# Performance work log

Measured on AMD Instinct MI355X. Metric: run time of the kernel, lower is better.

Reference implementation:

```python
import jax, jax.numpy as jnp
import numpy as np

N_NODES = 131072
N_EDGES = 2097152
N_GRAPHS = 2048
IN_CH, HID, OUT = 12, 64, 4


def gcn_conv(x, W, b, src, dst, n_nodes):
    """PyG GCNConv: out = D^{-1/2} (A + I) D^{-1/2} (x W) + b.
    Degree computed at target nodes including self loops (edge_weight=1)."""
    h = x @ W  # [N, F_out]
    # degree with self loops: in-degree + 1
    deg = jax.ops.segment_sum(jnp.ones((src.shape[0],), x.dtype), dst,
                              num_segments=n_nodes) + 1.0
    dinv = jax.lax.rsqrt(deg)  # [N]
    norm = dinv[src] * dinv[dst]  # [E]
    # scatter-add messages from src to dst
    agg = jax.ops.segment_sum(h[src] * norm[:, None], dst, num_segments=n_nodes)
    # self-loop contribution: norm_ii = dinv[i]^2
    agg = agg + h * (dinv * dinv)[:, None]
    return agg + b


def global_mean_pool(x, batch, n_graphs):
    sums = jax.ops.segment_sum(x, batch, num_segments=n_graphs)
    cnt = jax.ops.segment_sum(jnp.ones((x.shape[0],), x.dtype), batch,
                              num_segments=n_graphs)
    return sums / jnp.maximum(cnt, 1.0)[:, None]


def setup_inputs() -> dict:
    key = jax.random.key(0)
    ks = jax.random.split(key, 9)
    x = jax.random.normal(ks[0], (N_NODES, IN_CH), dtype=jnp.float32)
    edge_index = jax.random.randint(ks[1], (2, N_EDGES), 0, N_NODES, dtype=jnp.int64)
    batch = jnp.sort(jax.random.randint(ks[2], (N_NODES,), 0, N_GRAPHS, dtype=jnp.int64))
    def glorot(k, shape):
        lim = np.sqrt(6.0 / (shape[0] + shape[1]))
        return jax.random.uniform(k, shape, jnp.float32, -lim, lim)
    return {
        "x": x,
        "edge_index": edge_index,
        "batch": batch,
        "W1": glorot(ks[3], (IN_CH, HID)),
        "b1": jnp.zeros((HID,), jnp.float32),
        "W2": glorot(ks[4], (HID, HID)),
        "b2": jnp.zeros((HID,), jnp.float32),
        "Wfc": glorot(ks[5], (HID, OUT)),
        "bfc": jnp.zeros((OUT,), jnp.float32),
    }


def reference(x, edge_index, batch, W1, b1, W2, b2, Wfc, bfc):
    src, dst = edge_index[0], edge_index[1]
    h = jax.nn.relu(gcn_conv(x, W1, b1, src, dst, N_NODES))
    h = jax.nn.relu(gcn_conv(h, W2, b2, src, dst, N_NODES))
    g = global_mean_pool(h, batch, N_GRAPHS)  # [n_graphs, HID]
    return jax.nn.sigmoid(g @ Wfc + bfc)  # [n_graphs, OUT]
```

## Files before the change

### kernel.cpp

```cpp
#include <hip/hip_runtime.h>
#include <hip/hip_bf16.h>


#define N_NODES 131072
#define N_EDGES 2097152
#define N_GRAPHS 2048
#define IN_CH 12
#define HID 64
#define OUT_CH 4
#define NBUCK 512
#define CHUNK 8192
#define STRIDE 4608
#define CSR_STRIDE 5120
#define CAP 5120

typedef float f32x2 __attribute__((ext_vector_type(2)));

__device__ __forceinline__ unsigned short f2bf(float f) {
    unsigned u = __float_as_uint(f);
    return (unsigned short)((u + 0x7fffu + ((u >> 16) & 1u)) >> 16);
}
__device__ __forceinline__ unsigned pack2bf(float lo, float hi) {
    return (unsigned)f2bf(lo) | ((unsigned)f2bf(hi) << 16);
}
__device__ __forceinline__ float bflo(unsigned v) { return __uint_as_float(v << 16); }
__device__ __forceinline__ float bfhi(unsigned v) { return __uint_as_float(v & 0xFFFF0000u); }

__global__ __launch_bounds__(1024, 4)
void bucket_kernel(const int* __restrict__ src, const int* __restrict__ dst,
                   int* __restrict__ bucket_count, int* __restrict__ staged) {
    __shared__ int hist[NBUCK];
    __shared__ int lscan[NBUCK];
    __shared__ int gbase[NBUCK];
    __shared__ int cursor[NBUCK];
    __shared__ int sorted[CHUNK];
    int tid = threadIdx.x;
    int base = blockIdx.x * CHUNK;
    if (tid < NBUCK) { hist[tid] = 0; cursor[tid] = 0; }
    __syncthreads();
    int d8[8], s8[8];
#pragma unroll
    for (int k = 0; k < 8; k++) {
        int i = base + k * 1024 + tid;
        d8[k] = dst[i];
        s8[k] = src[i];
        atomicAdd(&hist[d8[k] >> 8], 1);
    }
    __syncthreads();
    if (tid < NBUCK) lscan[tid] = hist[tid];
    __syncthreads();
    for (int off = 1; off < NBUCK; off <<= 1) {
        int u = (tid < NBUCK && tid >= off) ? lscan[tid - off] : 0;
        __syncthreads();
        if (tid < NBUCK) lscan[tid] += u;
        __syncthreads();
    }
    if (tid < NBUCK) gbase[tid] = atomicAdd(&bucket_count[tid], hist[tid]);
    __syncthreads();
#pragma unroll
    for (int k = 0; k < 8; k++) {
        int b = d8[k] >> 8;
        int start = lscan[b] - hist[b];
        int p = start + atomicAdd(&cursor[b], 1);
        sorted[p] = ((d8[k] & 255) << 17) | s8[k];
    }
    __syncthreads();
    int wid = tid >> 6, lane = tid & 63;
    int g16 = lane >> 4, k16 = lane & 15;
    for (int b0 = wid * 4; b0 < NBUCK; b0 += 64) {
        int b = b0 + g16;
        int cb = hist[b];
        int lbase = lscan[b] - cb;
        int gb = b * STRIDE + gbase[b];
        for (int k = k16; k < cb; k += 16) staged[gb + k] = sorted[lbase + k];
    }
}

__global__ void build_kernel(const int* __restrict__ bucket_count, const int* __restrict__ staged,
                             int2* __restrict__ rowbounds, float* __restrict__ dinv,
                             int* __restrict__ csr, const float* __restrict__ x,
                             unsigned short* __restrict__ xb) {
    __shared__ int sl[STRIDE];
    __shared__ int image[CAP];
    __shared__ int cnt[256];
    __shared__ int scn[256];
    __shared__ int loff[256];
    __shared__ int cursor[256];
    __shared__ int totalS;
    int b = blockIdx.x;
    int tid = threadIdx.x;
    int count = bucket_count[b];
    const int* st = staged + b * STRIDE;
    cnt[tid] = 0;
    cursor[tid] = 0;
    for (int i = tid; i < count; i += 256) sl[i] = st[i];
    __syncthreads();
    for (int i = tid; i < count; i += 256) atomicAdd(&cnt[(sl[i] >> 17) & 255], 1);
    __syncthreads();
    int deg = cnt[tid];
    int degp = (deg + 3) & ~3;
    scn[tid] = degp;
    __syncthreads();
    for (int off = 1; off < 256; off <<= 1) {
        int u = (tid >= off) ? scn[tid - off] : 0;
        __syncthreads();
        scn[tid] += u;
        __syncthreads();
    }
    int lo = scn[tid] - degp;
    loff[tid] = lo;
    int nbase = (b << 8) + tid;
    int gb = b * CSR_STRIDE;
    rowbounds[nbase] = make_int2(gb + lo, gb + lo + degp);
    float dv = rsqrtf((float)deg + 1.0f);
    dinv[nbase] = dv;
    if (tid == 255) totalS = lo + degp;
    {
        const float* xp = x + nbase * IN_CH;
        unsigned o[8];
#pragma unroll
        for (int k = 0; k < 6; k++) o[k] = pack2bf(dv * xp[2 * k], dv * xp[2 * k + 1]);
        o[6] = 0; o[7] = 0;
        uint4* dstp = (uint4*)(xb + nbase * 16);
        dstp[0] = make_uint4(o[0], o[1], o[2], o[3]);
        dstp[1] = make_uint4(o[4], o[5], o[6], o[7]);
    }
    if (b == 0 && tid < 2)
        ((uint4*)(xb + (size_t)N_NODES * 16))[tid] = make_uint4(0, 0, 0, 0);
    __syncthreads();
    for (int i = tid; i < count; i += 256) {
        int rec = sl[i];
        int s = rec & 0x1FFFF;
        int dq = (rec >> 17) & 255;
        int p = loff[dq] + atomicAdd(&cursor[dq], 1);
        int val = s << 6;
        if (p < CAP) image[p] = val;
        else csr[gb + p] = val;
    }
    __syncthreads();
    int padval = N_NODES << 6;
    for (int p = loff[tid] + deg; p < loff[tid] + degp; p++) {
        if (p < CAP) image[p] = padval;
        else csr[gb + p] = padval;
    }
    __syncthreads();
    int lim = totalS < CAP ? totalS : CAP;
    int* dstp = csr + gb;
    for (int i = tid; i < lim; i += 256) dstp[i] = image[i];
}

__global__ void agg_x_kernel(const int2* __restrict__ rowbounds, const int* __restrict__ csr,
                             const float* __restrict__ dinv,
                             const unsigned short* __restrict__ xb, float* __restrict__ aggx) {
    int tid = threadIdx.x;
    int w = tid >> 6, lane = tid & 63, sub = lane >> 1, p = lane & 1;
    int qoff = 8 * p;
    int node = (blockIdx.x * 4 + w) * 32 + sub;
    int2 rb = rowbounds[node];
    float dn = dinv[node];
    f32x2 a0[4] = {{0, 0}, {0, 0}, {0, 0}, {0, 0}};
    f32x2 a1[4] = {{0, 0}, {0, 0}, {0, 0}, {0, 0}};
    f32x2 a2[4] = {{0, 0}, {0, 0}, {0, 0}, {0, 0}};
    f32x2 a3[4] = {{0, 0}, {0, 0}, {0, 0}, {0, 0}};
    for (int j = rb.x; j < rb.y; j += 4) {
        int4 e = *(const int4*)(csr + j);
        uint4 u0 = *(const uint4*)(xb + (e.x >> 2) + qoff);
        uint4 u1 = *(const uint4*)(xb + (e.y >> 2) + qoff);
        uint4 u2 = *(const uint4*)(xb + (e.z >> 2) + qoff);
        uint4 u3 = *(const uint4*)(xb + (e.w >> 2) + qoff);
        a0[0] += (f32x2){bflo(u0.x), bfhi(u0.x)};
        a0[1] += (f32x2){bflo(u0.y), bfhi(u0.y)};
        a0[2] += (f32x2){bflo(u0.z), bfhi(u0.z)};
        a0[3] += (f32x2){bflo(u0.w), bfhi(u0.w)};
        a1[0] += (f32x2){bflo(u1.x), bfhi(u1.x)};
        a1[1] += (f32x2){bflo(u1.y), bfhi(u1.y)};
        a1[2] += (f32x2){bflo(u1.z), bfhi(u1.z)};
        a1[3] += (f32x2){bflo(u1.w), bfhi(u1.w)};
        a2[0] += (f32x2){bflo(u2.x), bfhi(u2.x)};
        a2[1] += (f32x2){bflo(u2.y), bfhi(u2.y)};
        a2[2] += (f32x2){bflo(u2.z), bfhi(u2.z)};
        a2[3] += (f32x2){bflo(u2.w), bfhi(u2.w)};
        a3[0] += (f32x2){bflo(u3.x), bfhi(u3.x)};
        a3[1] += (f32x2){bflo(u3.y), bfhi(u3.y)};
        a3[2] += (f32x2){bflo(u3.z), bfhi(u3.z)};
        a3[3] += (f32x2){bflo(u3.w), bfhi(u3.w)};
    }
    uint4 su = *(const uint4*)(xb + node * 16 + qoff);
    a0[0] += (f32x2){bflo(su.x), bfhi(su.x)};
    a0[1] += (f32x2){bflo(su.y), bfhi(su.y)};
    a0[2] += (f32x2){bflo(su.z), bfhi(su.z)};
    a0[3] += (f32x2){bflo(su.w), bfhi(su.w)};
    f32x2 nd = {dn, dn};
    f32x2 s0 = nd * ((a0[0] + a1[0]) + (a2[0] + a3[0]));
    f32x2 s1 = nd * ((a0[1] + a1[1]) + (a2[1] + a3[1]));
    f32x2 s2 = nd * ((a0[2] + a1[2]) + (a2[2] + a3[2]));
    f32x2 s3 = nd * ((a0[3] + a1[3]) + (a2[3] + a3[3]));
    float4 o0 = make_float4(s0[0], s0[1], s1[0], s1[1]);
    float4 o1 = make_float4(s2[0], s2[1], s3[0], s3[1]);
    *(float4*)(aggx + node * 16 + qoff) = o0;
    *(float4*)(aggx + node * 16 + qoff + 4) = o1;
}

__global__ void w1w2_kernel(const float* __restrict__ aggx, const float* __restrict__ W1,
                            const float* __restrict__ b1, const float* __restrict__ W2,
                            const float* __restrict__ dinv, unsigned int* __restrict__ hout) {
    __shared__ float sW1[IN_CH * HID];
    __shared__ float sW2[HID * HID];
    __shared__ float sA[256];
    __shared__ float sh1[16 * HID];
    int tid = threadIdx.x;
    for (int i = tid; i < IN_CH * HID; i += 256) sW1[i] = W1[i];
    for (int i = tid; i < HID * HID; i += 256) sW2[i] = W2[i];
    int node0 = blockIdx.x * 16;
    sA[tid] = aggx[node0 * 16 + tid];
    __syncthreads();
    int nl = tid >> 4, c4 = (tid & 15) * 4;
    float a0 = 0, a1 = 0, a2 = 0, a3 = 0;
#pragma unroll
    for (int k = 0; k < IN_CH; k++) {
        float av = sA[nl * 16 + k];
        const float* w = &sW1[k * HID + c4];
        a0 += av * w[0]; a1 += av * w[1]; a2 += av * w[2]; a3 += av * w[3];
    }
    const float* bb = &b1[c4];
    sh1[nl * HID + c4 + 0] = fmaxf(a0 + bb[0], 0.0f);
    sh1[nl * HID + c4 + 1] = fmaxf(a1 + bb[1], 0.0f);
    sh1[nl * HID + c4 + 2] = fmaxf(a2 + bb[2], 0.0f);
    sh1[nl * HID + c4 + 3] = fmaxf(a3 + bb[3], 0.0f);
    __syncthreads();
    float c0 = 0, c1 = 0, c2 = 0, c3 = 0;
#pragma unroll 8
    for (int k = 0; k < HID; k++) {
        float hv = sh1[nl * HID + k];
        float4 w = *(const float4*)&sW2[k * HID + c4];
        c0 += hv * w.x; c1 += hv * w.y; c2 += hv * w.z; c3 += hv * w.w;
    }
    float dv = dinv[node0 + nl];
    unsigned int packed = (unsigned int)__builtin_amdgcn_cvt_pk_fp8_f32(dv * c0, dv * c1, 0, false);
    packed = (unsigned int)__builtin_amdgcn_cvt_pk_fp8_f32(dv * c2, dv * c3, (int)packed, true);
    hout[((node0 + nl) * HID + c4) >> 2] = packed;
    if (blockIdx.x == 0 && tid < 16)
        hout[((size_t)N_NODES * HID >> 2) + tid] = 0;
}

__device__ __forceinline__ void add_fp8(f32x2* a, uint2 u) {
    a[0] += __builtin_amdgcn_cvt_pk_f32_fp8((int)u.x, false);
    a[1] += __builtin_amdgcn_cvt_pk_f32_fp8((int)u.x, true);
    a[2] += __builtin_amdgcn_cvt_pk_f32_fp8((int)u.y, false);
    a[3] += __builtin_amdgcn_cvt_pk_f32_fp8((int)u.y, true);
}

__device__ __forceinline__ void agg_body(int beg, int end, const int* __restrict__ csr,
                                         const unsigned char* __restrict__ h,
                                         int qoff, float* r) {
    f32x2 a0[4] = {{0, 0}, {0, 0}, {0, 0}, {0, 0}};
    f32x2 a1[4] = {{0, 0}, {0, 0}, {0, 0}, {0, 0}};
    f32x2 a2[4] = {{0, 0}, {0, 0}, {0, 0}, {0, 0}};
    f32x2 a3[4] = {{0, 0}, {0, 0}, {0, 0}, {0, 0}};
    int j = beg;
    for (; j + 8 <= end; j += 8) {
        int4 ea = *(const int4*)(csr + j);
        int4 eb = *(const int4*)(csr + j + 4);
        uint2 u0 = *(const uint2*)(h + ea.x + qoff);
        uint2 u1 = *(const uint2*)(h + ea.y + qoff);
        uint2 u2 = *(const uint2*)(h + ea.z + qoff);
        uint2 u3 = *(const uint2*)(h + ea.w + qoff);
        uint2 u4 = *(const uint2*)(h + eb.x + qoff);
        uint2 u5 = *(const uint2*)(h + eb.y + qoff);
        uint2 u6 = *(const uint2*)(h + eb.z + qoff);
        uint2 u7 = *(const uint2*)(h + eb.w + qoff);
        add_fp8(a0, u0); add_fp8(a1, u1); add_fp8(a2, u2); add_fp8(a3, u3);
        add_fp8(a0, u4); add_fp8(a1, u5); add_fp8(a2, u6); add_fp8(a3, u7);
    }
    if (j < end) {
        int4 ea = *(const int4*)(csr + j);
        uint2 u0 = *(const uint2*)(h + ea.x + qoff);
        uint2 u1 = *(const uint2*)(h + ea.y + qoff);
        uint2 u2 = *(const uint2*)(h + ea.z + qoff);
        uint2 u3 = *(const uint2*)(h + ea.w + qoff);
        add_fp8(a0, u0); add_fp8(a1, u1); add_fp8(a2, u2); add_fp8(a3, u3);
    }
#pragma unroll
    for (int k = 0; k < 4; k++) {
        f32x2 s = (a0[k] + a1[k]) + (a2[k] + a3[k]);
        r[2 * k] = s[0];
        r[2 * k + 1] = s[1];
    }
}

__global__ void agg_pool_kernel(const int2* __restrict__ rowbounds, const int* __restrict__ csr,
                                const float* __restrict__ dinv,
                                const unsigned char* __restrict__ h,
                                const float* __restrict__ b, const int* __restrict__ batch,
                                float* __restrict__ pool, float* __restrict__ gcnt) {
    __shared__ float red[32][HID];
    __shared__ int gids[32];
    int tid = threadIdx.x;
    int w = tid >> 6, lane = tid & 63, sub = lane >> 3, q = lane & 7;
    int qoff = 8 * q;
    int node = (blockIdx.x * 4 + w) * 8 + sub;
    int2 rb = rowbounds[node];
    float dn = dinv[node];
    float r[8];
    agg_body(rb.x, rb.y, csr, h, qoff, r);
    uint2 su = *(const uint2*)(h + node * HID + qoff);
    f32x2 s0 = __builtin_amdgcn_cvt_pk_f32_fp8((int)su.x, false);
    f32x2 s1 = __builtin_amdgcn_cvt_pk_f32_fp8((int)su.x, true);
    f32x2 s2 = __builtin_amdgcn_cvt_pk_f32_fp8((int)su.y, false);
    f32x2 s3 = __builtin_amdgcn_cvt_pk_f32_fp8((int)su.y, true);
    float4 b0 = *(const float4*)&b[qoff];
    float4 b1 = *(const float4*)&b[qoff + 4];
    float4 v0, v1;
    v0.x = fmaxf(dn * (r[0] + s0[0]) + b0.x, 0.0f);
    v0.y = fmaxf(dn * (r[1] + s0[1]) + b0.y, 0.0f);
    v0.z = fmaxf(dn * (r[2] + s1[0]) + b0.z, 0.0f);
    v0.w = fmaxf(dn * (r[3] + s1[1]) + b0.w, 0.0f);
    v1.x = fmaxf(dn * (r[4] + s2[0]) + b1.x, 0.0f);
    v1.y = fmaxf(dn * (r[5] + s2[1]) + b1.y, 0.0f);
    v1.z = fmaxf(dn * (r[6] + s3[0]) + b1.z, 0.0f);
    v1.w = fmaxf(dn * (r[7] + s3[1]) + b1.w, 0.0f);
    int nl = w * 8 + sub;
    *(float4*)&red[nl][qoff] = v0;
    *(float4*)&red[nl][qoff + 4] = v1;
    if (q == 0) gids[nl] = batch[node];
    __syncthreads();
    if (tid < 64) {
        int c = tid;
        float acc = 0.0f;
        int cur = gids[0], cnt = 0;
        for (int n = 0; n < 32; n++) {
            int g = gids[n];
            if (g != cur) {
                atomicAdd(&pool[cur * HID + c], acc);
                if (c == 0) atomicAdd(&gcnt[cur], (float)cnt);
                acc = 0.0f; cnt = 0; cur = g;
            }
            acc += red[n][c];
            cnt++;
        }
        atomicAdd(&pool[cur * HID + c], acc);
        if (c == 0) atomicAdd(&gcnt[cur], (float)cnt);
    }
}

__global__ void final_kernel(const float* __restrict__ pool, const float* __restrict__ gcnt,
                             const float* __restrict__ Wfc, const float* __restrict__ bfc,
                             float* __restrict__ out) {
    int idx = blockIdx.x * 256 + threadIdx.x;
    if (idx >= N_GRAPHS * OUT_CH) return;
    int g = idx >> 2, o = idx & 3;
    float inv = 1.0f / fmaxf(gcnt[g], 1.0f);
    float acc = bfc[o];
#pragma unroll
    for (int k = 0; k < HID; k++) acc += pool[g * HID + k] * inv * Wfc[k * OUT_CH + o];
    out[idx] = 1.0f / (1.0f + expf(-acc));
}

extern "C" void kernel_launch(void* const* d_in, const int* in_sizes, int n_in,
                              void* d_out, int out_size, void* d_ws, size_t ws_size,
                              hipStream_t stream) {
    const float* x   = (const float*)d_in[0];
    const int* eidx  = (const int*)d_in[1];
    const int* batch = (const int*)d_in[2];
    const float* W1  = (const float*)d_in[3];
    const float* b1  = (const float*)d_in[4];
    const float* W2  = (const float*)d_in[5];
    const float* b2  = (const float*)d_in[6];
    const float* Wfc = (const float*)d_in[7];
    const float* bfc = (const float*)d_in[8];
    float* out = (float*)d_out;

    const int* src = eidx;
    const int* dst = eidx + N_EDGES;

    unsigned char* hB = (unsigned char*)d_ws;
    int*   csr    = (int*)(hB + (size_t)(N_NODES + 1) * HID);
    int*   staged = csr + (size_t)NBUCK * CSR_STRIDE;
    float* dinv   = (float*)(staged + (size_t)NBUCK * STRIDE);
    int2*  rowbounds = (int2*)(dinv + N_NODES);
    int*   bucket_count = (int*)(rowbounds + N_NODES);
    float* pool   = (float*)(bucket_count + NBUCK);
    float* gcnt   = pool + N_GRAPHS * HID;
    unsigned short* xb = (unsigned short*)(gcnt + N_GRAPHS);
    float* aggx   = (float*)(xb + (size_t)(N_NODES + 1) * 16);

    hipMemsetAsync(bucket_count, 0, (size_t)NBUCK * 4, stream);
    hipMemsetAsync(pool, 0, (size_t)(N_GRAPHS * HID + N_GRAPHS) * 4, stream);

    bucket_kernel<<<N_EDGES / CHUNK, 1024, 0, stream>>>(src, dst, bucket_count, staged);
    build_kernel<<<NBUCK, 256, 0, stream>>>(bucket_count, staged, rowbounds, dinv, csr, x, xb);

    agg_x_kernel<<<N_NODES / 128, 256, 0, stream>>>(rowbounds, csr, dinv, xb, aggx);
    w1w2_kernel<<<N_NODES / 16, 256, 0, stream>>>(aggx, W1, b1, W2, dinv, (unsigned int*)hB);

    agg_pool_kernel<<<N_NODES / 32, 256, 0, stream>>>(rowbounds, csr, dinv, hB, b2, batch,
                                                      pool, gcnt);

    final_kernel<<<(N_GRAPHS * OUT_CH + 255) / 256, 256, 0, stream>>>(pool, gcnt, Wfc, bfc, out);
}
```

Before: 197.1 us.

## Split fp8 hidden features into two channel halves aggregated in separate passes

The second-layer fp8 feature matrix is stored as two 32-channel planes instead of one 64-channel row, and aggregation plus pooling runs as two passes, one per half. Each pass gathers from a 4 MB table rather than an 8 MB one, so the random neighbour gathers are meant to hit in cache more often. In exchange the CSR indices and row bounds are read twice, pool atomics are split across two launches, and there is an extra kernel launch.

```diff
diff --git a/kernel.cpp b/kernel.cpp
--- a/kernel.cpp
+++ b/kernel.cpp
@@ -203,7 +203,8 @@
 
 __global__ void w1w2_kernel(const float* __restrict__ aggx, const float* __restrict__ W1,
                             const float* __restrict__ b1, const float* __restrict__ W2,
-                            const float* __restrict__ dinv, unsigned int* __restrict__ hout) {
+                            const float* __restrict__ dinv,
+                            unsigned char* __restrict__ hBa, unsigned char* __restrict__ hBb) {
     __shared__ float sW1[IN_CH * HID];
     __shared__ float sW2[HID * HID];
     __shared__ float sA[256];
@@ -238,9 +239,12 @@
     float dv = dinv[node0 + nl];
     unsigned int packed = (unsigned int)__builtin_amdgcn_cvt_pk_fp8_f32(dv * c0, dv * c1, 0, false);
     packed = (unsigned int)__builtin_amdgcn_cvt_pk_fp8_f32(dv * c2, dv * c3, (int)packed, true);
-    hout[((node0 + nl) * HID + c4) >> 2] = packed;
-    if (blockIdx.x == 0 && tid < 16)
-        hout[((size_t)N_NODES * HID >> 2) + tid] = 0;
+    unsigned char* base = (c4 < 32) ? hBa : hBb;
+    *(unsigned int*)(base + (size_t)(node0 + nl) * 32 + (c4 & 31)) = packed;
+    if (blockIdx.x == 0 && tid < 8) {
+        ((unsigned int*)(hBa + (size_t)N_NODES * 32))[tid] = 0;
+        ((unsigned int*)(hBb + (size_t)N_NODES * 32))[tid] = 0;
+    }
 }
 
 __device__ __forceinline__ void add_fp8(f32x2* a, uint2 u) {
@@ -250,96 +254,88 @@
     a[3] += __builtin_amdgcn_cvt_pk_f32_fp8((int)u.y, true);
 }
 
-__device__ __forceinline__ void agg_body(int beg, int end, const int* __restrict__ csr,
-                                         const unsigned char* __restrict__ h,
-                                         int qoff, float* r) {
+__global__ void agg_pool_half_kernel(const int2* __restrict__ rowbounds,
+                                     const int* __restrict__ csr,
+                                     const float* __restrict__ dinv,
+                                     const unsigned char* __restrict__ h,
+                                     const float* __restrict__ b2,
+                                     const int* __restrict__ batch,
+                                     float* __restrict__ pool, float* __restrict__ gcnt,
+                                     int chan_off, int do_gcnt) {
+    __shared__ float red[64][32];
+    __shared__ int gids[64];
+    int tid = threadIdx.x;
+    int w = tid >> 6, lane = tid & 63, sub = lane >> 2, q = lane & 3;
+    int qoff = 8 * q;
+    int nl = w * 16 + sub;
+    int node = blockIdx.x * 64 + nl;
+    int2 rb = rowbounds[node];
+    float dn = dinv[node];
     f32x2 a0[4] = {{0, 0}, {0, 0}, {0, 0}, {0, 0}};
     f32x2 a1[4] = {{0, 0}, {0, 0}, {0, 0}, {0, 0}};
     f32x2 a2[4] = {{0, 0}, {0, 0}, {0, 0}, {0, 0}};
     f32x2 a3[4] = {{0, 0}, {0, 0}, {0, 0}, {0, 0}};
-    int j = beg;
-    for (; j + 8 <= end; j += 8) {
+    int j = rb.x;
+    for (; j + 8 <= rb.y; j += 8) {
         int4 ea = *(const int4*)(csr + j);
         int4 eb = *(const int4*)(csr + j + 4);
-        uint2 u0 = *(const uint2*)(h + ea.x + qoff);
-        uint2 u1 = *(const uint2*)(h + ea.y + qoff);
-        uint2 u2 = *(const uint2*)(h + ea.z + qoff);
-        uint2 u3 = *(const uint2*)(h + ea.w + qoff);
-        uint2 u4 = *(const uint2*)(h + eb.x + qoff);
-        uint2 u5 = *(const uint2*)(h + eb.y + qoff);
-        uint2 u6 = *(const uint2*)(h + eb.z + qoff);
-        uint2 u7 = *(const uint2*)(h + eb.w + qoff);
+        uint2 u0 = *(const uint2*)(h + (ea.x >> 1) + qoff);
+        uint2 u1 = *(const uint2*)(h + (ea.y >> 1) + qoff);
+        uint2 u2 = *(const uint2*)(h + (ea.z >> 1) + qoff);
+        uint2 u3 = *(const uint2*)(h + (ea.w >> 1) + qoff);
+        uint2 u4 = *(const uint2*)(h + (eb.x >> 1) + qoff);
+        uint2 u5 = *(const uint2*)(h + (eb.y >> 1) + qoff);
+        uint2 u6 = *(const uint2*)(h + (eb.z >> 1) + qoff);
+        uint2 u7 = *(const uint2*)(h + (eb.w >> 1) + qoff);
         add_fp8(a0, u0); add_fp8(a1, u1); add_fp8(a2, u2); add_fp8(a3, u3);
         add_fp8(a0, u4); add_fp8(a1, u5); add_fp8(a2, u6); add_fp8(a3, u7);
     }
-    if (j < end) {
+    if (j < rb.y) {
         int4 ea = *(const int4*)(csr + j);
-        uint2 u0 = *(const uint2*)(h + ea.x + qoff);
-        uint2 u1 = *(const uint2*)(h + ea.y + qoff);
-        uint2 u2 = *(const uint2*)(h + ea.z + qoff);
-        uint2 u3 = *(const uint2*)(h + ea.w + qoff);
+        uint2 u0 = *(const uint2*)(h + (ea.x >> 1) + qoff);
+        uint2 u1 = *(const uint2*)(h + (ea.y >> 1) + qoff);
+        uint2 u2 = *(const uint2*)(h + (ea.z >> 1) + qoff);
+        uint2 u3 = *(const uint2*)(h + (ea.w >> 1) + qoff);
         add_fp8(a0, u0); add_fp8(a1, u1); add_fp8(a2, u2); add_fp8(a3, u3);
     }
-#pragma unroll
-    for (int k = 0; k < 4; k++) {
-        f32x2 s = (a0[k] + a1[k]) + (a2[k] + a3[k]);
-        r[2 * k] = s[0];
-        r[2 * k + 1] = s[1];
-    }
-}
-
-__global__ void agg_pool_kernel(const int2* __restrict__ rowbounds, const int* __restrict__ csr,
-                                const float* __restrict__ dinv,
-                                const unsigned char* __restrict__ h,
-                                const float* __restrict__ b, const int* __restrict__ batch,
-                                float* __restrict__ pool, float* __restrict__ gcnt) {
-    __shared__ float red[32][HID];
-    __shared__ int gids[32];
-    int tid = threadIdx.x;
-    int w = tid >> 6, lane = tid & 63, sub = lane >> 3, q = lane & 7;
-    int qoff = 8 * q;
-    int node = (blockIdx.x * 4 + w) * 8 + sub;
-    int2 rb = rowbounds[node];
-    float dn = dinv[node];
-    float r[8];
-    agg_body(rb.x, rb.y, csr, h, qoff, r);
-    uint2 su = *(const uint2*)(h + node * HID + qoff);
-    f32x2 s0 = __builtin_amdgcn_cvt_pk_f32_fp8((int)su.x, false);
-    f32x2 s1 = __builtin_amdgcn_cvt_pk_f32_fp8((int)su.x, true);
-    f32x2 s2 = __builtin_amdgcn_cvt_pk_f32_fp8((int)su.y, false);
-    f32x2 s3 = __builtin_amdgcn_cvt_pk_f32_fp8((int)su.y, true);
-    float4 b0 = *(const float4*)&b[qoff];
-    float4 b1 = *(const float4*)&b[qoff + 4];
+    uint2 su = *(const uint2*)(h + (size_t)node * 32 + qoff);
+    add_fp8(a0, su);
+    f32x2 s0 = (a0[0] + a1[0]) + (a2[0] + a3[0]);
+    f32x2 s1 = (a0[1] + a1[1]) + (a2[1] + a3[1]);
+    f32x2 s2 = (a0[2] + a1[2]) + (a2[2] + a3[2]);
+    f32x2 s3 = (a0[3] + a1[3]) + (a2[3] + a3[3]);
+    float4 bb0 = *(const float4*)&b2[chan_off + qoff];
+    float4 bb1 = *(const float4*)&b2[chan_off + qoff + 4];
     float4 v0, v1;
-    v0.x = fmaxf(dn * (r[0] + s0[0]) + b0.x, 0.0f);
-    v0.y = fmaxf(dn * (r[1] + s0[1]) + b0.y, 0.0f);
-    v0.z = fmaxf(dn * (r[2] + s1[0]) + b0.z, 0.0f);
-    v0.w = fmaxf(dn * (r[3] + s1[1]) + b0.w, 0.0f);
-    v1.x = fmaxf(dn * (r[4] + s2[0]) + b1.x, 0.0f);
-    v1.y = fmaxf(dn * (r[5] + s2[1]) + b1.y, 0.0f);
-    v1.z = fmaxf(dn * (r[6] + s3[0]) + b1.z, 0.0f);
-    v1.w = fmaxf(dn * (r[7] + s3[1]) + b1.w, 0.0f);
-    int nl = w * 8 + sub;
+    v0.x = fmaxf(dn * s0[0] + bb0.x, 0.0f);
+    v0.y = fmaxf(dn * s0[1] + bb0.y, 0.0f);
+    v0.z = fmaxf(dn * s1[0] + bb0.z, 0.0f);
+    v0.w = fmaxf(dn * s1[1] + bb0.w, 0.0f);
+    v1.x = fmaxf(dn * s2[0] + bb1.x, 0.0f);
+    v1.y = fmaxf(dn * s2[1] + bb1.y, 0.0f);
+    v1.z = fmaxf(dn * s3[0] + bb1.z, 0.0f);
+    v1.w = fmaxf(dn * s3[1] + bb1.w, 0.0f);
     *(float4*)&red[nl][qoff] = v0;
     *(float4*)&red[nl][qoff + 4] = v1;
     if (q == 0) gids[nl] = batch[node];
     __syncthreads();
     if (tid < 64) {
-        int c = tid;
+        int half = tid >> 5, c = tid & 31;
+        int n0 = half * 32;
         float acc = 0.0f;
-        int cur = gids[0], cnt = 0;
-        for (int n = 0; n < 32; n++) {
+        int cur = gids[n0], cnt = 0;
+        for (int n = n0; n < n0 + 32; n++) {
             int g = gids[n];
             if (g != cur) {
-                atomicAdd(&pool[cur * HID + c], acc);
-                if (c == 0) atomicAdd(&gcnt[cur], (float)cnt);
+                atomicAdd(&pool[cur * HID + chan_off + c], acc);
+                if (do_gcnt && c == 0) atomicAdd(&gcnt[cur], (float)cnt);
                 acc = 0.0f; cnt = 0; cur = g;
             }
             acc += red[n][c];
             cnt++;
         }
-        atomicAdd(&pool[cur * HID + c], acc);
-        if (c == 0) atomicAdd(&gcnt[cur], (float)cnt);
+        atomicAdd(&pool[cur * HID + chan_off + c], acc);
+        if (do_gcnt && c == 0) atomicAdd(&gcnt[cur], (float)cnt);
     }
 }
 
@@ -373,8 +369,9 @@
     const int* src = eidx;
     const int* dst = eidx + N_EDGES;
 
-    unsigned char* hB = (unsigned char*)d_ws;
-    int*   csr    = (int*)(hB + (size_t)(N_NODES + 1) * HID);
+    unsigned char* hBa = (unsigned char*)d_ws;
+    unsigned char* hBb = hBa + (size_t)(N_NODES + 1) * 32;
+    int*   csr    = (int*)(hBb + (size_t)(N_NODES + 1) * 32);
     int*   staged = csr + (size_t)NBUCK * CSR_STRIDE;
     float* dinv   = (float*)(staged + (size_t)NBUCK * STRIDE);
     int2*  rowbounds = (int2*)(dinv + N_NODES);
@@ -391,10 +388,12 @@
     build_kernel<<<NBUCK, 256, 0, stream>>>(bucket_count, staged, rowbounds, dinv, csr, x, xb);
 
     agg_x_kernel<<<N_NODES / 128, 256, 0, stream>>>(rowbounds, csr, dinv, xb, aggx);
-    w1w2_kernel<<<N_NODES / 16, 256, 0, stream>>>(aggx, W1, b1, W2, dinv, (unsigned int*)hB);
-
-    agg_pool_kernel<<<N_NODES / 32, 256, 0, stream>>>(rowbounds, csr, dinv, hB, b2, batch,
-                                                      pool, gcnt);
+    w1w2_kernel<<<N_NODES / 16, 256, 0, stream>>>(aggx, W1, b1, W2, dinv, hBa, hBb);
+
+    agg_pool_half_kernel<<<N_NODES / 64, 256, 0, stream>>>(rowbounds, csr, dinv, hBa, b2,
+                                                           batch, pool, gcnt, 0, 1);
+    agg_pool_half_kernel<<<N_NODES / 64, 256, 0, stream>>>(rowbounds, csr, dinv, hBb, b2,
+                                                           batch, pool, gcnt, 32, 0);
 
     final_kernel<<<(N_GRAPHS * OUT_CH + 255) / 256, 256, 0, stream>>>(pool, gcnt, Wfc, bfc, out);
 }
```

New measurement: 211.0 us. 1.07x slower.

## Process 64 nodes per block in w1w2 kernel with register-tiled 4x4 matmul

Applied to the files above, without the earlier changes.

The dense W1/W2 kernel now handles 64 nodes per block instead of 16, so the shared-memory load of the W1/W2 weights is spread over four times as many nodes. Each thread computes a 4-node by 4-channel tile of the second matmul from float4 loads, and the hidden layer is stored transposed with padding to avoid bank conflicts. This reduces redundant weight staging and LDS traffic per FMA. In exchange it uses more shared memory per block and more registers, which may lower occupancy.

```diff
diff --git a/kernel.cpp b/kernel.cpp
--- a/kernel.cpp
+++ b/kernel.cpp
@@ -206,41 +206,68 @@
                             const float* __restrict__ dinv, unsigned int* __restrict__ hout) {
     __shared__ float sW1[IN_CH * HID];
     __shared__ float sW2[HID * HID];
-    __shared__ float sA[256];
-    __shared__ float sh1[16 * HID];
+    __shared__ float sA[64 * 17];
+    __shared__ float sh1t[HID * 65];
     int tid = threadIdx.x;
     for (int i = tid; i < IN_CH * HID; i += 256) sW1[i] = W1[i];
     for (int i = tid; i < HID * HID; i += 256) sW2[i] = W2[i];
-    int node0 = blockIdx.x * 16;
-    sA[tid] = aggx[node0 * 16 + tid];
-    __syncthreads();
-    int nl = tid >> 4, c4 = (tid & 15) * 4;
-    float a0 = 0, a1 = 0, a2 = 0, a3 = 0;
-#pragma unroll
-    for (int k = 0; k < IN_CH; k++) {
-        float av = sA[nl * 16 + k];
-        const float* w = &sW1[k * HID + c4];
-        a0 += av * w[0]; a1 += av * w[1]; a2 += av * w[2]; a3 += av * w[3];
-    }
-    const float* bb = &b1[c4];
-    sh1[nl * HID + c4 + 0] = fmaxf(a0 + bb[0], 0.0f);
-    sh1[nl * HID + c4 + 1] = fmaxf(a1 + bb[1], 0.0f);
-    sh1[nl * HID + c4 + 2] = fmaxf(a2 + bb[2], 0.0f);
-    sh1[nl * HID + c4 + 3] = fmaxf(a3 + bb[3], 0.0f);
-    __syncthreads();
-    float c0 = 0, c1 = 0, c2 = 0, c3 = 0;
-#pragma unroll 8
+    int node0 = blockIdx.x * 64;
+    {
+        float4 v = *(const float4*)(aggx + node0 * 16 + tid * 4);
+        int n = tid >> 2, part = (tid & 3) * 4;
+        sA[n * 17 + part + 0] = v.x;
+        sA[n * 17 + part + 1] = v.y;
+        sA[n * 17 + part + 2] = v.z;
+        sA[n * 17 + part + 3] = v.w;
+    }
+    __syncthreads();
+    int w = tid >> 6, c = tid & 63;
+    float bc = b1[c];
+#pragma unroll
+    for (int it = 0; it < 4; it++) {
+        int n0 = w * 16 + it * 4;
+        float a0 = bc, a1 = bc, a2 = bc, a3 = bc;
+#pragma unroll
+        for (int k = 0; k < IN_CH; k++) {
+            float wv = sW1[k * HID + c];
+            a0 += sA[(n0 + 0) * 17 + k] * wv;
+            a1 += sA[(n0 + 1) * 17 + k] * wv;
+            a2 += sA[(n0 + 2) * 17 + k] * wv;
+            a3 += sA[(n0 + 3) * 17 + k] * wv;
+        }
+        float4 o = make_float4(fmaxf(a0, 0.0f), fmaxf(a1, 0.0f),
+                               fmaxf(a2, 0.0f), fmaxf(a3, 0.0f));
+        *(float4*)&sh1t[c * 65 + n0] = o;
+    }
+    __syncthreads();
+    int nq = tid >> 4, c4 = (tid & 15) * 4;
+    float4 a0 = {0, 0, 0, 0}, a1 = {0, 0, 0, 0}, a2 = {0, 0, 0, 0}, a3 = {0, 0, 0, 0};
+#pragma unroll 4
     for (int k = 0; k < HID; k++) {
-        float hv = sh1[nl * HID + k];
-        float4 w = *(const float4*)&sW2[k * HID + c4];
-        c0 += hv * w.x; c1 += hv * w.y; c2 += hv * w.z; c3 += hv * w.w;
-    }
-    float dv = dinv[node0 + nl];
-    unsigned int packed = (unsigned int)__builtin_amdgcn_cvt_pk_fp8_f32(dv * c0, dv * c1, 0, false);
-    packed = (unsigned int)__builtin_amdgcn_cvt_pk_fp8_f32(dv * c2, dv * c3, (int)packed, true);
-    hout[((node0 + nl) * HID + c4) >> 2] = packed;
+        float4 wv = *(const float4*)&sW2[k * HID + c4];
+        float4 hv = *(const float4*)&sh1t[k * 65 + nq * 4];
+        a0.x += hv.x * wv.x; a0.y += hv.x * wv.y; a0.z += hv.x * wv.z; a0.w += hv.x * wv.w;
+        a1.x += hv.y * wv.x; a1.y += hv.y * wv.y; a1.z += hv.y * wv.z; a1.w += hv.y * wv.w;
+        a2.x += hv.z * wv.x; a2.y += hv.z * wv.y; a2.z += hv.z * wv.z; a2.w += hv.z * wv.w;
+        a3.x += hv.w * wv.x; a3.y += hv.w * wv.y; a3.z += hv.w * wv.z; a3.w += hv.w * wv.w;
+    }
+    int nb = node0 + nq * 4;
+    float dv0 = dinv[nb + 0], dv1 = dinv[nb + 1], dv2 = dinv[nb + 2], dv3 = dinv[nb + 3];
+    unsigned int p0 = (unsigned int)__builtin_amdgcn_cvt_pk_fp8_f32(dv0 * a0.x, dv0 * a0.y, 0, false);
+    p0 = (unsigned int)__builtin_amdgcn_cvt_pk_fp8_f32(dv0 * a0.z, dv0 * a0.w, (int)p0, true);
+    unsigned int p1 = (unsigned int)__builtin_amdgcn_cvt_pk_fp8_f32(dv1 * a1.x, dv1 * a1.y, 0, false);
+    p1 = (unsigned int)__builtin_amdgcn_cvt_pk_fp8_f32(dv1 * a1.z, dv1 * a1.w, (int)p1, true);
+    unsigned int p2 = (unsigned int)__builtin_amdgcn_cvt_pk_fp8_f32(dv2 * a2.x, dv2 * a2.y, 0, false);
+    p2 = (unsigned int)__builtin_amdgcn_cvt_pk_fp8_f32(dv2 * a2.z, dv2 * a2.w, (int)p2, true);
+    unsigned int p3 = (unsigned int)__builtin_amdgcn_cvt_pk_fp8_f32(dv3 * a3.x, dv3 * a3.y, 0, false);
+    p3 = (unsigned int)__builtin_amdgcn_cvt_pk_fp8_f32(dv3 * a3.z, dv3 * a3.w, (int)p3, true);
+    int cl = c4 >> 2;
+    hout[(nb + 0) * 16 + cl] = p0;
+    hout[(nb + 1) * 16 + cl] = p1;
+    hout[(nb + 2) * 16 + cl] = p2;
+    hout[(nb + 3) * 16 + cl] = p3;
     if (blockIdx.x == 0 && tid < 16)
-        hout[((size_t)N_NODES * HID >> 2) + tid] = 0;
+        hout[(size_t)N_NODES * 16 + tid] = 0;
 }
 
 __device__ __forceinline__ void add_fp8(f32x2* a, uint2 u) {
@@ -391,7 +418,7 @@
     build_kernel<<<NBUCK, 256, 0, stream>>>(bucket_count, staged, rowbounds, dinv, csr, x, xb);
 
     agg_x_kernel<<<N_NODES / 128, 256, 0, stream>>>(rowbounds, csr, dinv, xb, aggx);
-    w1w2_kernel<<<N_NODES / 16, 256, 0, stream>>>(aggx, W1, b1, W2, dinv, (unsigned int*)hB);
+    w1w2_kernel<<<N_NODES / 64, 256, 0, stream>>>(aggx, W1, b1, W2, dinv, (unsigned int*)hB);
 
     agg_pool_kernel<<<N_NODES / 32, 256, 0, stream>>>(rowbounds, csr, dinv, hB, b2, batch,
                                                       pool, gcnt);
```

Result: faster. 192.0 us (-2.6%).
